# Performance work log

Measured on AMD Instinct MI355X. Metric: run time of the kernel, lower is better.

Reference implementation:

```python
import jax, jax.numpy as jnp
import numpy as np
from jax import lax

SCALE = 2
NUM_POINTS = 4

def conv2d(x, w, b, pad):
    # x: [B,C,H,W], w: [O,I,kh,kw]
    y = lax.conv_general_dilated(x, w, (1, 1), [(pad, pad), (pad, pad)],
                                 dimension_numbers=("NCHW", "OIHW", "NCHW"))
    return y + b[None, :, None, None]

def grid_sample_border(feat, grid):
    # feat: [B,C,H,W]; grid: [B,Hg,Wg,2] in [-1,1] (x,y), align_corners=False,
    # padding_mode='border' (coordinates clipped before interpolation, as in torch).
    B, C, H, W = feat.shape
    Hg, Wg = grid.shape[1], grid.shape[2]
    gx = jnp.clip((grid[..., 0] + 1.0) * W / 2.0 - 0.5, 0.0, W - 1.0)
    gy = jnp.clip((grid[..., 1] + 1.0) * H / 2.0 - 0.5, 0.0, H - 1.0)
    x0 = jnp.floor(gx); y0 = jnp.floor(gy)
    fx = (gx - x0).reshape(B, 1, -1)
    fy = (gy - y0).reshape(B, 1, -1)
    x0i = jnp.clip(x0.astype(jnp.int32), 0, W - 1)
    y0i = jnp.clip(y0.astype(jnp.int32), 0, H - 1)
    x1i = jnp.clip(x0i + 1, 0, W - 1)
    y1i = jnp.clip(y0i + 1, 0, H - 1)
    featf = feat.reshape(B, C, H * W)
    def gather(yi, xi):
        idx = (yi * W + xi).reshape(B, 1, -1)
        return jnp.take_along_axis(featf, idx, axis=2)  # [B,C,Hg*Wg]
    v00 = gather(y0i, x0i); v01 = gather(y0i, x1i)
    v10 = gather(y1i, x0i); v11 = gather(y1i, x1i)
    out = (v00 * (1 - fx) * (1 - fy) + v01 * fx * (1 - fy)
           + v10 * (1 - fx) * fy + v11 * fx * fy)
    return out.reshape(B, C, Hg, Wg)

def setup_inputs() -> dict:
    key = jax.random.key(0)
    ks = jax.random.split(key, 8)
    B, Cin, Cout, H, W = 8, 256, 256, 64, 64
    high_feat = jax.random.normal(ks[0], (B, Cin, H, W), jnp.float32)
    low_feat = jax.random.normal(ks[1], (B, Cout, H * SCALE, W * SCALE), jnp.float32)
    W1 = jax.random.normal(ks[2], (Cin, Cin + Cout, 1, 1), jnp.float32) * 0.02
    b1 = jnp.zeros((Cin,), jnp.float32)
    # original inits offset_conv2 to zeros; use small random to exercise deformable sampling
    W2 = jax.random.normal(ks[3], (NUM_POINTS * 2, Cin, 3, 3), jnp.float32) * 0.01
    b2 = jnp.zeros((NUM_POINTS * 2,), jnp.float32)
    Wf = jax.random.normal(ks[4], (Cout, Cin, 1, 1), jnp.float32) * 0.05
    bf = jnp.zeros((Cout,), jnp.float32)
    return {"high_feat": high_feat, "low_feat": low_feat, "W1": W1, "b1": b1,
            "W2": W2, "b2": b2, "Wf": Wf, "bf": bf}

def reference(high_feat, low_feat, W1, b1, W2, b2, Wf, bf):
    B, Cin, H, W = high_feat.shape
    H_up, W_up = H * SCALE, W * SCALE
    # bilinear upsample, align_corners=False (half-pixel centers)
    up_high = jax.image.resize(high_feat, (B, Cin, H_up, W_up), method="bilinear")
    concat = jnp.concatenate([up_high, low_feat], axis=1)
    off_feat = jax.nn.relu(conv2d(concat, W1, b1, 0))
    offsets = conv2d(off_feat, W2, b2, 1)  # [B, 2P, H_up, W_up]
    proc = conv2d(high_feat, Wf, bf, 0)    # [B, Cout, H, W]
    # base grid in [-1,1], (x,y)
    gy = jnp.linspace(-1.0, 1.0, H_up)
    gx = jnp.linspace(-1.0, 1.0, W_up)
    base = jnp.stack(jnp.meshgrid(gx, gy, indexing="xy"), axis=-1)  # [H_up,W_up,2]
    # offsets -> [B,P,2,H,W] -> [P,B,H,W,2], normalized to [-1,1] units
    off = offsets.reshape(B, NUM_POINTS, 2, H_up, W_up).transpose(1, 0, 3, 4, 2)
    norm = jnp.array([W_up, H_up], jnp.float32)
    off = off / norm * 2.0
    grids = base[None, None] + off  # [P,B,H_up,W_up,2]
    sampled = jax.vmap(lambda g: grid_sample_border(proc, g))(grids)  # [P,B,C,H_up,W_up]
    return jnp.mean(sampled, axis=0)
```

## Files before the change

kernel.cpp:

```cpp
#include <hip/hip_runtime.h>
#include <stdint.h>

#define NB   8
#define CH   256
#define HW0  4096
#define HW2  16384

typedef __attribute__((ext_vector_type(8))) short short8;
typedef __attribute__((ext_vector_type(8))) unsigned short u16x8;
typedef __attribute__((ext_vector_type(4))) unsigned short u16x4;
typedef __attribute__((ext_vector_type(4))) float floatx4;

__device__ inline unsigned short f2bf(float f) {
    union { float f; uint32_t u; } v; v.f = f;
    return (unsigned short)((v.u + 0x7FFFu + ((v.u >> 16) & 1u)) >> 16);
}
__device__ inline float bf2f(unsigned short h) {
    union { uint32_t u; float f; } v; v.u = ((uint32_t)h) << 16;
    return v.f;
}

__global__ __launch_bounds__(256) void ktrans(const float* __restrict__ src,
        unsigned short* __restrict__ dst, int M) {
    const int b = blockIdx.z, k0 = blockIdx.y * 32, m0 = blockIdx.x * 128;
    const int tid = threadIdx.x;
    __shared__ unsigned short tile[32][132];
    const float* s = src + ((size_t)b * CH + k0) * M + m0;
    for (int c = tid; c < 1024; c += 256) {
        int kk = c >> 5, mm = (c & 31) * 4;
        float4 v = *(const float4*)(s + (size_t)kk * M + mm);
        u16x4 o = { f2bf(v.x), f2bf(v.y), f2bf(v.z), f2bf(v.w) };
        *(u16x4*)&tile[kk][mm] = o;
    }
    __syncthreads();
    unsigned short* d = dst + ((size_t)b * M + m0) * CH + k0;
    for (int c = tid; c < 512; c += 256) {
        int mm = c >> 2, kc = (c & 3) * 8;
        u16x8 v;
        #pragma unroll
        for (int i = 0; i < 8; ++i) v[i] = tile[kc + i][mm];
        *(u16x8*)(d + (size_t)mm * CH + kc) = v;
    }
}

__global__ __launch_bounds__(256) void kwconv(const float* __restrict__ W1,
        const float* __restrict__ Wf, unsigned short* __restrict__ A1,
        unsigned short* __restrict__ A2) {
    int i = blockIdx.x * 256 + threadIdx.x;
    if (i < 512 * 256) {
        int n = i >> 8, k = i & 255;
        float v = (n < 256) ? W1[n * 512 + k] : Wf[(size_t)(n - 256) * 256 + k];
        A1[i] = f2bf(v);
    }
    if (i < 256 * 256) {
        int n = i >> 8, k = i & 255;
        A2[i] = f2bf(W1[n * 512 + 256 + k]);
    }
}

__global__ __launch_bounds__(256) void kwpack(const float* __restrict__ W2v,
        unsigned short* __restrict__ W3p) {
    int i = blockIdx.x * 256 + threadIdx.x;
    if (i >= 9 * 16 * 256) return;
    int ci = i & 255, o = (i >> 8) & 15, t = i >> 12;
    float v = (o < 8) ? W2v[((size_t)o * 256 + ci) * 9 + t] : 0.0f;
    W3p[i] = f2bf(v);
}

__global__ __launch_bounds__(256) void k1_mfma(
    const unsigned short* __restrict__ highT,
    const unsigned short* __restrict__ A1,
    const float* __restrict__ bfv,
    float* __restrict__ T, float* __restrict__ procT)
{
    const int b = blockIdx.z;
    const int m0 = blockIdx.x * 128;
    const int n0 = blockIdx.y * 128;
    const int tid = threadIdx.x;
    __shared__ __attribute__((aligned(16))) unsigned short smem[2 * 128 * 40];
    unsigned short* As = smem;
    unsigned short* Xs = smem + 128 * 40;
    const int lane = tid & 63, wid = tid >> 6;
    const int wn = (wid >> 1) * 64, wm = (wid & 1) * 64;
    const int l15 = lane & 15, quad = lane >> 4;

    floatx4 acc[4][4];
    #pragma unroll
    for (int i = 0; i < 4; ++i)
        #pragma unroll
        for (int j = 0; j < 4; ++j)
            acc[i][j] = (floatx4){0.f, 0.f, 0.f, 0.f};

    const unsigned short* Xg = highT + ((size_t)b * HW0 + m0) * CH;

    for (int k0 = 0; k0 < 256; k0 += 32) {
        for (int c = tid; c < 512; c += 256) {
            int row = c >> 2, kc = (c & 3) * 8;
            *(u16x8*)&As[row * 40 + kc] =
                *(const u16x8*)(A1 + (size_t)(n0 + row) * CH + k0 + kc);
            *(u16x8*)&Xs[row * 40 + kc] =
                *(const u16x8*)(Xg + (size_t)row * CH + k0 + kc);
        }
        __syncthreads();
        short8 af[4], bfr[4];
        #pragma unroll
        for (int i = 0; i < 4; ++i)
            af[i] = *(const short8*)&As[(wn + i * 16 + l15) * 40 + quad * 8];
        #pragma unroll
        for (int j = 0; j < 4; ++j)
            bfr[j] = *(const short8*)&Xs[(wm + j * 16 + l15) * 40 + quad * 8];
        #pragma unroll
        for (int i = 0; i < 4; ++i)
            #pragma unroll
            for (int j = 0; j < 4; ++j)
                acc[i][j] = __builtin_amdgcn_mfma_f32_16x16x32_bf16(
                    af[i], bfr[j], acc[i][j], 0, 0, 0);
        __syncthreads();
    }

    if (n0 < 256) {
        #pragma unroll
        for (int i = 0; i < 4; ++i) {
            int nb = n0 + wn + i * 16 + quad * 4;
            #pragma unroll
            for (int r = 0; r < 4; ++r) {
                int n = nb + r;
                #pragma unroll
                for (int j = 0; j < 4; ++j) {
                    int m = m0 + wm + j * 16 + l15;
                    T[((size_t)b * CH + n) * HW0 + m] = acc[i][j][r];
                }
            }
        }
    } else {
        float* tf = (float*)smem;
        const int nc = n0 - 256;
        #pragma unroll
        for (int mq = 0; mq < 4; ++mq) {
            __syncthreads();
            if ((wid & 1) == (mq >> 1)) {
                #pragma unroll
                for (int jj = 0; jj < 2; ++jj) {
                    int j = (mq & 1) * 2 + jj;
                    int ml = j * 16 + l15 - (mq & 1) * 32;
                    #pragma unroll
                    for (int i = 0; i < 4; ++i) {
                        int nl = wn + i * 16 + quad * 4;
                        #pragma unroll
                        for (int r = 0; r < 4; ++r)
                            tf[ml * 132 + nl + r] = acc[i][j][r] + bfv[nc + nl + r];
                    }
                }
            }
            __syncthreads();
            int mm = tid >> 3;
            int c8 = tid & 7;
            float* dst = procT + ((size_t)b * HW0 + m0 + mq * 32 + mm) * CH + nc;
            #pragma unroll
            for (int k = 0; k < 4; ++k) {
                int col = c8 * 4 + k * 32;
                *(float4*)(dst + col) = *(const float4*)&tf[mm * 132 + col];
            }
        }
    }
}

__global__ __launch_bounds__(256) void k2_mfma(
    const unsigned short* __restrict__ lowT,
    const unsigned short* __restrict__ A2,
    const float* __restrict__ b1, const float* __restrict__ T,
    unsigned short* __restrict__ off_featT)
{
    const int b = blockIdx.z;
    const int m0 = blockIdx.x * 128;
    const int n0 = blockIdx.y * 128;
    const int tid = threadIdx.x;
    __shared__ unsigned short smem[2 * 128 * 40];
    unsigned short* As = smem;
    unsigned short* Xs = smem + 128 * 40;
    const int lane = tid & 63, wid = tid >> 6;
    const int wn = (wid >> 1) * 64, wm = (wid & 1) * 64;
    const int l15 = lane & 15, quad = lane >> 4;

    floatx4 acc[4][4];
    #pragma unroll
    for (int i = 0; i < 4; ++i)
        #pragma unroll
        for (int j = 0; j < 4; ++j)
            acc[i][j] = (floatx4){0.f, 0.f, 0.f, 0.f};

    const unsigned short* Xg = lowT + ((size_t)b * HW2 + m0) * CH;

    for (int k0 = 0; k0 < 256; k0 += 32) {
        for (int c = tid; c < 512; c += 256) {
            int row = c >> 2, kc = (c & 3) * 8;
            *(u16x8*)&As[row * 40 + kc] =
                *(const u16x8*)(A2 + (size_t)(n0 + row) * CH + k0 + kc);
            *(u16x8*)&Xs[row * 40 + kc] =
                *(const u16x8*)(Xg + (size_t)row * CH + k0 + kc);
        }
        __syncthreads();
        short8 af[4], bfr[4];
        #pragma unroll
        for (int i = 0; i < 4; ++i)
            af[i] = *(const short8*)&As[(wn + i * 16 + l15) * 40 + quad * 8];
        #pragma unroll
        for (int j = 0; j < 4; ++j)
            bfr[j] = *(const short8*)&Xs[(wm + j * 16 + l15) * 40 + quad * 8];
        #pragma unroll
        for (int i = 0; i < 4; ++i)
            #pragma unroll
            for (int j = 0; j < 4; ++j)
                acc[i][j] = __builtin_amdgcn_mfma_f32_16x16x32_bf16(
                    af[i], bfr[j], acc[i][j], 0, 0, 0);
        __syncthreads();
    }

    const int y = blockIdx.x;
    int hk = y >> 1;
    int yA, yB; float wyA, wyB;
    if (y & 1) { yA = hk; yB = min(hk + 1, 63); wyA = 0.75f; wyB = 0.25f; }
    else       { yB = hk; yA = max(hk - 1, 0);  wyA = 0.25f; wyB = 0.75f; }

    int xA[4], xB[4]; float wxA[4], wxB[4];
    #pragma unroll
    for (int j = 0; j < 4; ++j) {
        int x = wm + j * 16 + l15;
        int xk = x >> 1;
        if (x & 1) { xA[j] = xk; xB[j] = min(xk + 1, 63); wxA[j] = 0.75f; wxB[j] = 0.25f; }
        else       { xB[j] = xk; xA[j] = max(xk - 1, 0);  wxA[j] = 0.25f; wxB[j] = 0.75f; }
    }

    #pragma unroll
    for (int i = 0; i < 4; ++i) {
        int nb = n0 + wn + i * 16 + quad * 4;
        #pragma unroll
        for (int r = 0; r < 4; ++r) {
            int n = nb + r;
            const float* tb  = T + ((size_t)b * CH + n) * HW0;
            const float* trA = tb + yA * 64;
            const float* trB = tb + yB * 64;
            float bias = b1[n];
            #pragma unroll
            for (int j = 0; j < 4; ++j) {
                float up = wyA * (wxA[j] * trA[xA[j]] + wxB[j] * trA[xB[j]])
                         + wyB * (wxA[j] * trB[xA[j]] + wxB[j] * trB[xB[j]]);
                acc[i][j][r] = fmaxf(acc[i][j][r] + up + bias, 0.0f);
            }
        }
    }

    unsigned short (*tile)[136] = (unsigned short (*)[136])smem;
    for (int xh = 0; xh < 2; ++xh) {
        __syncthreads();
        if ((wid & 1) == xh) {
            #pragma unroll
            for (int i = 0; i < 4; ++i) {
                int nc = wn + i * 16 + quad * 4;
                #pragma unroll
                for (int j = 0; j < 4; ++j) {
                    int xr = j * 16 + l15;
                    unsigned int lo = (unsigned int)f2bf(acc[i][j][0])
                                    | ((unsigned int)f2bf(acc[i][j][1]) << 16);
                    unsigned int hi = (unsigned int)f2bf(acc[i][j][2])
                                    | ((unsigned int)f2bf(acc[i][j][3]) << 16);
                    *(unsigned int*)&tile[xr][nc]     = lo;
                    *(unsigned int*)&tile[xr][nc + 2] = hi;
                }
            }
        }
        __syncthreads();
        for (int c = tid; c < 1024; c += 256) {
            int xr = c >> 4, nc = (c & 15) * 8;
            u16x8 v = *(u16x8*)&tile[xr][nc];
            *(u16x8*)(off_featT +
                ((size_t)b * HW2 + (size_t)y * 128 + xh * 64 + xr) * CH + n0 + nc) = v;
        }
    }
}

__global__ __launch_bounds__(256) void k3_mfma(
    const unsigned short* __restrict__ offT,
    const unsigned short* __restrict__ W3p,
    float* __restrict__ offs)
{
    const int b = blockIdx.y;
    const int y = blockIdx.x;
    const int tid = threadIdx.x;
    const int lane = tid & 63, w = tid >> 6;
    const int l15 = lane & 15, quad = lane >> 4;

    floatx4 acc[2];
    acc[0] = (floatx4){0.f, 0.f, 0.f, 0.f};
    acc[1] = (floatx4){0.f, 0.f, 0.f, 0.f};

    const unsigned short* xb = offT + (size_t)b * HW2 * CH;
    const int xbase = w * 32 + l15;

    for (int k0 = 0; k0 < 256; k0 += 32) {
        #pragma unroll
        for (int t = 0; t < 9; ++t) {
            const int dy = t / 3 - 1, dx = t % 3 - 1;
            const int yy = y + dy;
            if ((unsigned)yy >= 128u) continue;
            short8 bw = *(const short8*)(W3p + (size_t)(t * 16 + l15) * CH
                                         + k0 + quad * 8);
            const unsigned short* rowp = xb + ((size_t)yy * 128) * CH + k0 + quad * 8;
            #pragma unroll
            for (int j = 0; j < 2; ++j) {
                int xx = xbase + j * 16 + dx;
                short8 ax = (short8){0, 0, 0, 0, 0, 0, 0, 0};
                if ((unsigned)xx < 128u)
                    ax = *(const short8*)(rowp + (size_t)xx * CH);
                acc[j] = __builtin_amdgcn_mfma_f32_16x16x32_bf16(
                    ax, bw, acc[j], 0, 0, 0);
            }
        }
    }

    if (l15 < 8) {
        float* ob = offs + ((size_t)b * 8 + l15) * HW2 + (size_t)y * 128;
        #pragma unroll
        for (int j = 0; j < 2; ++j) {
            int xpix = w * 32 + j * 16 + quad * 4;
            *(floatx4*)(ob + xpix) = acc[j];
        }
    }
}

__global__ __launch_bounds__(256) void k4_sample(
    const float* __restrict__ offs, const float* __restrict__ b2v,
    const float* __restrict__ procT, float* __restrict__ out)
{
    const int blk = blockIdx.x;
    const int b  = blk & 7;
    const int r  = blk >> 3;
    const int y  = r >> 1;
    const int xh = r & 1;
    const int tid = threadIdx.x;
    const int lane = tid & 63, w = tid >> 6;

    __shared__ int2   sp_i[4][64];
    __shared__ float4 sp_w[4][64];
    __shared__ float  tile[4][8 * 260];

    if (tid < 64) {
        int x = xh * 64 + tid;
        float gxb = (2.0f * x) / 127.0f - 1.0f;
        float gyb = (2.0f * y) / 127.0f - 1.0f;
        const float* ob = offs + (size_t)b * 8 * HW2 + y * 128 + x;
        #pragma unroll
        for (int p = 0; p < 4; ++p) {
            float ox = ob[(2 * p) * HW2] + b2v[2 * p];
            float oy = ob[(2 * p + 1) * HW2] + b2v[2 * p + 1];
            float gx = gxb + ox * (2.0f / 128.0f);
            float gy = gyb + oy * (2.0f / 128.0f);
            float gxp = fminf(fmaxf((gx + 1.0f) * 32.0f - 0.5f, 0.0f), 63.0f);
            float gyp = fminf(fmaxf((gy + 1.0f) * 32.0f - 0.5f, 0.0f), 63.0f);
            float x0f = floorf(gxp), y0f = floorf(gyp);
            int x0 = (int)x0f, y0 = (int)y0f;
            int idx = (y0 * 64 + x0) * 256;
            int dxo = (x0 < 63) ? 256 : 0;
            int dyo = (y0 < 63) ? 16384 : 0;
            float fx = gxp - x0f, fy = gyp - y0f;
            float ex = 1.0f - fx, ey = 1.0f - fy;
            sp_i[p][tid] = make_int2(idx, dxo | (dyo << 16));
            sp_w[p][tid] = make_float4(0.25f * ex * ey, 0.25f * fx * ey,
                                       0.25f * ex * fy, 0.25f * fx * fy);
        }
    }
    __syncthreads();

    const float* P = procT + (size_t)b * HW0 * CH + lane * 4;
    float* tw = &tile[w][0];
    float* outb = out + (size_t)b * CH * HW2 + (size_t)y * 128 + xh * 64 + w * 16;

    for (int c8 = 0; c8 < 2; ++c8) {
        #pragma unroll
        for (int i = 0; i < 8; ++i) {
            int lpx = w * 16 + c8 * 8 + i;
            float4 a = make_float4(0.f, 0.f, 0.f, 0.f);
            #pragma unroll
            for (int p = 0; p < 4; ++p) {
                int2 si = sp_i[p][lpx];
                float4 sw = sp_w[p][lpx];
                int dxo = si.y & 0xFFFF, dyo = si.y >> 16;
                const float* q = P + si.x;
                float4 v00 = *(const float4*)(q);
                float4 v01 = *(const float4*)(q + dxo);
                float4 v10 = *(const float4*)(q + dyo);
                float4 v11 = *(const float4*)(q + dyo + dxo);
                a.x += sw.x * v00.x + sw.y * v01.x + sw.z * v10.x + sw.w * v11.x;
                a.y += sw.x * v00.y + sw.y * v01.y + sw.z * v10.y + sw.w * v11.y;
                a.z += sw.x * v00.z + sw.y * v01.z + sw.z * v10.z + sw.w * v11.z;
                a.w += sw.x * v00.w + sw.y * v01.w + sw.z * v10.w + sw.w * v11.w;
            }
            *(float4*)&tw[i * 260 + lane * 4] = a;
        }
        __syncthreads();
        #pragma unroll
        for (int g = 0; g < 32; ++g) {
            int c   = g * 8 + (lane >> 3);
            int pxl = lane & 7;
            outb[(size_t)c * HW2 + c8 * 8 + pxl] = tw[pxl * 260 + c];
        }
        __syncthreads();
    }
}

extern "C" void kernel_launch(void* const* d_in, const int* in_sizes, int n_in,
                              void* d_out, int out_size, void* d_ws, size_t ws_size,
                              hipStream_t stream) {
    const float* high = (const float*)d_in[0];
    const float* low  = (const float*)d_in[1];
    const float* W1   = (const float*)d_in[2];
    const float* b1   = (const float*)d_in[3];
    const float* W2v  = (const float*)d_in[4];
    const float* b2v  = (const float*)d_in[5];
    const float* Wf   = (const float*)d_in[6];
    const float* bfv  = (const float*)d_in[7];
    float* out = (float*)d_out;
    float* ws  = (float*)d_ws;

    float* T     = ws;
    float* procT = ws + 8388608;
    float* offs  = ws + 16777216;
    unsigned short* highT = (unsigned short*)(ws + 17825792);
    unsigned short* A1 = highT + 8388608;
    unsigned short* A2 = A1 + 131072;

    unsigned short* W3p = highT;

    unsigned short* lowT      = (unsigned short*)out;
    unsigned short* off_featT = ((unsigned short*)out) + 33554432;

    ktrans<<<dim3(32, 8, NB), 256, 0, stream>>>(high, highT, HW0);
    ktrans<<<dim3(128, 8, NB), 256, 0, stream>>>(low, lowT, HW2);
    kwconv<<<dim3(512), 256, 0, stream>>>(W1, Wf, A1, A2);

    k1_mfma<<<dim3(32, 4, NB), 256, 0, stream>>>(highT, A1, bfv, T, procT);
    kwpack<<<dim3(144), 256, 0, stream>>>(W2v, W3p);
    k2_mfma<<<dim3(128, 2, NB), 256, 0, stream>>>(lowT, A2, b1, T, off_featT);
    k3_mfma<<<dim3(128, NB), 256, 0, stream>>>(off_featT, W3p, offs);
    k4_sample<<<dim3(2048), 256, 0, stream>>>(offs, b2v, procT, out);
}
```

Baseline: 540.2 us.

## Fuse low_feat transpose into k2 and tile 3x3 conv through shared memory

The separate ktrans pass over low_feat is removed. k2 now reads fp32 NCHW low_feat directly, converts it to bf16 and writes it into the shared-memory tile, which saves a full write and re-read of a transposed copy. k3 is restructured to stage a 3-row halo tile in XOR-swizzled LDS, keep its weights in registers, split the K dimension across waves and reduce the partial sums through LDS. The grid is also raised from 1024 to 4096 blocks. Block indices are flattened with batch in the low bits across k1, k2 and k3, which changes the order blocks are scheduled in. The k2 loads from NCHW are strided per channel, and the larger LDS footprint in k3 may limit how many blocks fit per compute unit.

After: 512.0 us. -5.2%, faster.

```diff
diff --git a/kernel.cpp b/kernel.cpp
--- a/kernel.cpp
+++ b/kernel.cpp
@@ -73,9 +73,11 @@
     const float* __restrict__ bfv,
     float* __restrict__ T, float* __restrict__ procT)
 {
-    const int b = blockIdx.z;
-    const int m0 = blockIdx.x * 128;
-    const int n0 = blockIdx.y * 128;
+    const int bid = blockIdx.x;
+    const int b  = bid & 7;
+    const int q  = bid >> 3;
+    const int m0 = (q & 31) * 128;
+    const int n0 = (q >> 5) * 128;
     const int tid = threadIdx.x;
     __shared__ __attribute__((aligned(16))) unsigned short smem[2 * 128 * 40];
     unsigned short* As = smem;
@@ -166,14 +168,16 @@
 }
 
 __global__ __launch_bounds__(256) void k2_mfma(
-    const unsigned short* __restrict__ lowT,
+    const float* __restrict__ low,
     const unsigned short* __restrict__ A2,
     const float* __restrict__ b1, const float* __restrict__ T,
     unsigned short* __restrict__ off_featT)
 {
-    const int b = blockIdx.z;
-    const int m0 = blockIdx.x * 128;
-    const int n0 = blockIdx.y * 128;
+    const int bid = blockIdx.x;
+    const int b  = bid & 7;
+    const int q  = bid >> 3;
+    const int y  = q >> 1;
+    const int n0 = (q & 1) * 128;
     const int tid = threadIdx.x;
     __shared__ unsigned short smem[2 * 128 * 40];
     unsigned short* As = smem;
@@ -189,15 +193,25 @@
         for (int j = 0; j < 4; ++j)
             acc[i][j] = (floatx4){0.f, 0.f, 0.f, 0.f};
 
-    const unsigned short* Xg = lowT + ((size_t)b * HW2 + m0) * CH;
+    const float* Lg = low + (size_t)b * CH * HW2 + (size_t)y * 128;
+    const int spx = tid & 127, sg = tid >> 7;
 
     for (int k0 = 0; k0 < 256; k0 += 32) {
         for (int c = tid; c < 512; c += 256) {
             int row = c >> 2, kc = (c & 3) * 8;
             *(u16x8*)&As[row * 40 + kc] =
                 *(const u16x8*)(A2 + (size_t)(n0 + row) * CH + k0 + kc);
-            *(u16x8*)&Xs[row * 40 + kc] =
-                *(const u16x8*)(Xg + (size_t)row * CH + k0 + kc);
+        }
+        #pragma unroll
+        for (int itc = 0; itc < 4; ++itc) {
+            int cg4 = sg + itc * 2;
+            const float* lp = Lg + (size_t)(k0 + cg4 * 4) * HW2 + spx;
+            float v0 = lp[0];
+            float v1 = lp[HW2];
+            float v2 = lp[2 * HW2];
+            float v3 = lp[3 * HW2];
+            u16x4 o = { f2bf(v0), f2bf(v1), f2bf(v2), f2bf(v3) };
+            *(u16x4*)&Xs[spx * 40 + cg4 * 4] = o;
         }
         __syncthreads();
         short8 af[4], bfr[4];
@@ -216,7 +230,6 @@
         __syncthreads();
     }
 
-    const int y = blockIdx.x;
     int hk = y >> 1;
     int yA, yB; float wyA, wyB;
     if (y & 1) { yA = hk; yB = min(hk + 1, 63); wyA = 0.75f; wyB = 0.25f; }
@@ -284,48 +297,73 @@
     const unsigned short* __restrict__ W3p,
     float* __restrict__ offs)
 {
-    const int b = blockIdx.y;
-    const int y = blockIdx.x;
+    const int bid = blockIdx.x;
+    const int b  = bid & 7;
+    const int q  = bid >> 3;
+    const int y  = q >> 2;
+    const int xq = q & 3;
     const int tid = threadIdx.x;
     const int lane = tid & 63, w = tid >> 6;
     const int l15 = lane & 15, quad = lane >> 4;
 
+    __shared__ __attribute__((aligned(16))) unsigned short st[3 * 34 * 256];
+
+    short8 bw[9][2];
+    #pragma unroll
+    for (int t = 0; t < 9; ++t)
+        #pragma unroll
+        for (int k0 = 0; k0 < 2; ++k0)
+            bw[t][k0] = *(const short8*)(W3p + (size_t)(t * 16 + l15) * CH
+                                         + w * 64 + k0 * 32 + quad * 8);
+
+    const unsigned short* src = offT + (size_t)b * HW2 * CH;
+    for (int it = tid; it < 3264; it += 256) {
+        int s   = it & 31;
+        int px  = (it >> 5) % 34;
+        int row = it / (34 * 32);
+        int gy = y - 1 + row;
+        int gx = xq * 32 - 1 + px;
+        u16x8 v = (u16x8){0, 0, 0, 0, 0, 0, 0, 0};
+        if ((unsigned)gy < 128u && (unsigned)gx < 128u)
+            v = *(const u16x8*)(src + ((size_t)gy * 128 + gx) * CH + s * 8);
+        *(u16x8*)&st[(row * 34 + px) * 256 + ((s ^ (px & 7)) * 8)] = v;
+    }
+    __syncthreads();
+
     floatx4 acc[2];
     acc[0] = (floatx4){0.f, 0.f, 0.f, 0.f};
     acc[1] = (floatx4){0.f, 0.f, 0.f, 0.f};
 
-    const unsigned short* xb = offT + (size_t)b * HW2 * CH;
-    const int xbase = w * 32 + l15;
-
-    for (int k0 = 0; k0 < 256; k0 += 32) {
+    #pragma unroll
+    for (int k0 = 0; k0 < 2; ++k0) {
         #pragma unroll
         for (int t = 0; t < 9; ++t) {
-            const int dy = t / 3 - 1, dx = t % 3 - 1;
-            const int yy = y + dy;
-            if ((unsigned)yy >= 128u) continue;
-            short8 bw = *(const short8*)(W3p + (size_t)(t * 16 + l15) * CH
-                                         + k0 + quad * 8);
-            const unsigned short* rowp = xb + ((size_t)yy * 128) * CH + k0 + quad * 8;
+            const int row = t / 3, dxi = t % 3;
+            const int srd = w * 8 + k0 * 4 + quad;
             #pragma unroll
             for (int j = 0; j < 2; ++j) {
-                int xx = xbase + j * 16 + dx;
-                short8 ax = (short8){0, 0, 0, 0, 0, 0, 0, 0};
-                if ((unsigned)xx < 128u)
-                    ax = *(const short8*)(rowp + (size_t)xx * CH);
+                int px = j * 16 + l15 + dxi;
+                short8 a = *(const short8*)&st[(row * 34 + px) * 256
+                                               + ((srd ^ (px & 7)) * 8)];
                 acc[j] = __builtin_amdgcn_mfma_f32_16x16x32_bf16(
-                    ax, bw, acc[j], 0, 0, 0);
-            }
-        }
-    }
-
-    if (l15 < 8) {
-        float* ob = offs + ((size_t)b * 8 + l15) * HW2 + (size_t)y * 128;
-        #pragma unroll
-        for (int j = 0; j < 2; ++j) {
-            int xpix = w * 32 + j * 16 + quad * 4;
-            *(floatx4*)(ob + xpix) = acc[j];
-        }
-    }
+                    a, bw[t][k0], acc[j], 0, 0, 0);
+            }
+        }
+    }
+
+    __syncthreads();
+    float* red = (float*)st;
+    #pragma unroll
+    for (int j = 0; j < 2; ++j)
+        #pragma unroll
+        for (int r = 0; r < 4; ++r)
+            red[(w * 32 + j * 16 + quad * 4 + r) * 16 + l15] = acc[j][r];
+    __syncthreads();
+
+    const int oc = tid >> 5, px = tid & 31;
+    float s0 = red[px * 16 + oc]        + red[(32 + px) * 16 + oc]
+             + red[(64 + px) * 16 + oc] + red[(96 + px) * 16 + oc];
+    offs[((size_t)b * 8 + oc) * HW2 + (size_t)y * 128 + xq * 32 + px] = s0;
 }
 
 __global__ __launch_bounds__(256) void k4_sample(
@@ -385,11 +423,11 @@
                 int2 si = sp_i[p][lpx];
                 float4 sw = sp_w[p][lpx];
                 int dxo = si.y & 0xFFFF, dyo = si.y >> 16;
-                const float* q = P + si.x;
-                float4 v00 = *(const float4*)(q);
-                float4 v01 = *(const float4*)(q + dxo);
-                float4 v10 = *(const float4*)(q + dyo);
-                float4 v11 = *(const float4*)(q + dyo + dxo);
+                const float* qp = P + si.x;
+                float4 v00 = *(const float4*)(qp);
+                float4 v01 = *(const float4*)(qp + dxo);
+                float4 v10 = *(const float4*)(qp + dyo);
+                float4 v11 = *(const float4*)(qp + dyo + dxo);
                 a.x += sw.x * v00.x + sw.y * v01.x + sw.z * v10.x + sw.w * v11.x;
                 a.y += sw.x * v00.y + sw.y * v01.y + sw.z * v10.y + sw.w * v11.y;
                 a.z += sw.x * v00.z + sw.y * v01.z + sw.z * v10.z + sw.w * v11.z;
@@ -431,16 +469,14 @@
 
     unsigned short* W3p = highT;
 
-    unsigned short* lowT      = (unsigned short*)out;
     unsigned short* off_featT = ((unsigned short*)out) + 33554432;
 
     ktrans<<<dim3(32, 8, NB), 256, 0, stream>>>(high, highT, HW0);
-    ktrans<<<dim3(128, 8, NB), 256, 0, stream>>>(low, lowT, HW2);
     kwconv<<<dim3(512), 256, 0, stream>>>(W1, Wf, A1, A2);
 
-    k1_mfma<<<dim3(32, 4, NB), 256, 0, stream>>>(highT, A1, bfv, T, procT);
+    k1_mfma<<<dim3(1024), 256, 0, stream>>>(highT, A1, bfv, T, procT);
     kwpack<<<dim3(144), 256, 0, stream>>>(W2v, W3p);
-    k2_mfma<<<dim3(128, 2, NB), 256, 0, stream>>>(lowT, A2, b1, T, off_featT);
-    k3_mfma<<<dim3(128, NB), 256, 0, stream>>>(off_featT, W3p, offs);
+    k2_mfma<<<dim3(2048), 256, 0, stream>>>(low, A2, b1, T, off_featT);
+    k3_mfma<<<dim3(4096), 256, 0, stream>>>(off_featT, W3p, offs);
     k4_sample<<<dim3(2048), 256, 0, stream>>>(offs, b2v, procT, out);
 }
```
